# Kernel optimization log

Measured on AMD Instinct MI355X. Metric: run time of the kernel, lower is better.

Reference implementation:

```python
import jax, jax.numpy as jnp
import numpy as np

NUM_HEADS = 8
HEAD_DIM = 64
EMBED = NUM_HEADS * HEAD_DIM  # 512


def setup_inputs() -> dict:
    key = jax.random.key(0)
    ks = jax.random.split(key, 8)
    B, S = 4, 2048
    s = 1.0 / np.sqrt(HEAD_DIM)
    so = 1.0 / np.sqrt(EMBED)
    return {
        "queries": jax.random.normal(ks[0], (B, S, EMBED), jnp.float32),
        "keys": jax.random.normal(ks[1], (B, S, EMBED), jnp.float32),
        "values": jax.random.normal(ks[2], (B, S, EMBED), jnp.float32),
        "Wq": jax.random.uniform(ks[3], (HEAD_DIM, HEAD_DIM), jnp.float32, -s, s),
        "Wk": jax.random.uniform(ks[4], (HEAD_DIM, HEAD_DIM), jnp.float32, -s, s),
        "Wv": jax.random.uniform(ks[5], (HEAD_DIM, HEAD_DIM), jnp.float32, -s, s),
        "Wo": jax.random.uniform(ks[6], (EMBED, EMBED), jnp.float32, -so, so),
        "bo": jax.random.uniform(ks[7], (EMBED,), jnp.float32, -so, so),
    }


def reference(queries, keys, values, Wq, Wk, Wv, Wo, bo):
    B, Sq, _ = queries.shape
    # Faithful to source: keys/values are (buggily) reshaped from `queries`;
    # with equal seq lens this means k/v come from the queries tensor.
    q = queries.reshape(B, Sq, NUM_HEADS, HEAD_DIM)
    k = q
    v = q
    # per-head linear: torch Linear(x) = x @ W.T
    q = jnp.einsum('bshd,ed->bshe', q, Wq)
    k = jnp.einsum('bshd,ed->bshe', k, Wk)
    v = jnp.einsum('bshd,ed->bshe', v, Wv)
    sim = jnp.einsum('bqhd,bkhd->bhqk', q, k)  # [B,H,Sq,Sk]
    attn = jax.nn.softmax(sim * (1.0 / np.sqrt(HEAD_DIM)), axis=-1)
    out = jnp.einsum('bhqk,bkhd->bqhd', attn, v)
    out = out.reshape(B, Sq, EMBED)
    return out @ Wo.T + bo
```

## Files before the change

### kernel.cpp

```cpp
#include <hip/hip_runtime.h>
#include <cstddef>

#define S_ 2048
#define E_ 512
#define SPLIT_STRIDE 4194304u

typedef __attribute__((ext_vector_type(8)))  short bf16x8;
typedef __attribute__((ext_vector_type(16))) float f32x16;

__device__ __forceinline__ unsigned short f2bf(float f) {
    union { float f; unsigned u; } v; v.f = f;
    return (unsigned short)((v.u + 0x7FFFu + ((v.u >> 16) & 1u)) >> 16);
}
__device__ __forceinline__ unsigned pk2bf(float a, float b) {
    union { float f; unsigned u; } x, y; x.f = a; y.f = b;
    return __builtin_amdgcn_perm(y.u + 0x8000u, x.u + 0x8000u, 0x07060302u);
}
__device__ __forceinline__ float bflo(unsigned u) {
    union { unsigned u; float f; } v; v.u = u << 16; return v.f;
}
__device__ __forceinline__ float bfhi(unsigned u) {
    union { unsigned u; float f; } v; v.u = u & 0xffff0000u; return v.f;
}
__device__ __forceinline__ float fexp2(float x) {
#if __has_builtin(__builtin_amdgcn_exp2f)
    return __builtin_amdgcn_exp2f(x);
#else
    return exp2f(x);
#endif
}

__global__ __launch_bounds__(256) void prep_all(const float* __restrict__ X,
                                                const float* __restrict__ Wq,
                                                const float* __restrict__ Wk,
                                                const float* __restrict__ Wo,
                                                const float* __restrict__ Wv,
                                                unsigned short* __restrict__ Xbf,
                                                unsigned short* __restrict__ XTg,
                                                unsigned short* __restrict__ GT,
                                                unsigned short* __restrict__ W2) {
    __shared__ unsigned short T[64][72];
    const int bi = blockIdx.x, tid = threadIdx.x;
    if (bi < 1024) {
        const int st = bi & 31, h = (bi >> 5) & 7, b = bi >> 8;
        const int s0 = st * 64;
        const int j = tid >> 2, g = tid & 3;
        const float* src = X + ((size_t)(b * S_ + s0 + j) * E_) + h * 64 + g * 16;
        unsigned short us[16];
#pragma unroll
        for (int i = 0; i < 16; i += 4) {
            float4 f = *(const float4*)(src + i);
            us[i] = f2bf(f.x); us[i + 1] = f2bf(f.y);
            us[i + 2] = f2bf(f.z); us[i + 3] = f2bf(f.w);
        }
        size_t xb = ((size_t)(b * S_ + s0 + j) * E_) + h * 64 + g * 16;
        *(uint4*)&Xbf[xb]     = *(uint4*)&us[0];
        *(uint4*)&Xbf[xb + 8] = *(uint4*)&us[8];
#pragma unroll
        for (int i = 0; i < 16; ++i) T[g * 16 + i][j] = us[i];
        __syncthreads();
        const int d = tid >> 2;
        const int pm[16] = {0,1,2,3,8,9,10,11,4,5,6,7,12,13,14,15};
        unsigned short o[16];
#pragma unroll
        for (int i = 0; i < 16; ++i) o[i] = T[d][g * 16 + pm[i]];
        size_t tb = ((size_t)((b * 8 + h) * 64 + d)) * S_ + s0 + g * 16;
        *(uint4*)&XTg[tb]     = *(uint4*)&o[0];
        *(uint4*)&XTg[tb + 8] = *(uint4*)&o[8];
    } else if (bi < 1040) {
        int idx = (bi - 1024) * 256 + tid;
        int c = idx >> 6, d = idx & 63;
        float acc = 0.f;
#pragma unroll 8
        for (int e = 0; e < 64; ++e) acc += Wq[e * 64 + d] * Wk[e * 64 + c];
        GT[c * 64 + d] = f2bf(acc * 0.18033688011112042f);
    } else {
        int idx = (bi - 1040) * 256 + tid;
        int e = idx >> 9, f = idx & 511;
        int h = f >> 6, c = f & 63;
        const float* wo = Wo + e * 512 + h * 64;
        float acc = 0.f;
#pragma unroll 8
        for (int d = 0; d < 64; ++d) acc += wo[d] * Wv[d * 64 + c];
        W2[idx] = f2bf(acc);
    }
}

__global__ __launch_bounds__(256, 4) void attn_mfma(const unsigned short* __restrict__ Xbf,
                                                    const unsigned short* __restrict__ XTg,
                                                    const unsigned short* __restrict__ GT,
                                                    unsigned short* __restrict__ AOp,
                                                    float* __restrict__ Lp) {
    __shared__ union SM {
        unsigned short Q[128][72];
        unsigned short cbuf[2][2 * 64 * 72];
        unsigned short AOt[128][72];
    } sm;

    const int tid = threadIdx.x;
    const int w = tid >> 6, lane = tid & 63;
    const int lm = lane & 31, lh = lane >> 5;
    const int h = blockIdx.x & 7;
    const int rest = blockIdx.x >> 3;
    const int qt = rest & 15, b = (rest >> 4) & 3, split = rest >> 6;
    const int s0 = qt * 128, sk0 = split * (S_ / 2);

    {
        const int r = tid >> 1, c = (tid & 1) * 32;
        const unsigned short* src = Xbf + ((size_t)(b * S_ + s0 + r)) * E_ + h * 64 + c;
#pragma unroll
        for (int u = 0; u < 4; ++u) *(uint4*)&sm.Q[r][c + u * 8] = *(const uint4*)(src + u * 8);
    }
    __syncthreads();

    bf16x8 Ufrag[4];
    {
        f32x16 ua[2];
#pragma unroll
        for (int nt = 0; nt < 2; ++nt)
#pragma unroll
            for (int i = 0; i < 16; ++i) ua[nt][i] = 0.f;
#pragma unroll
        for (int ks = 0; ks < 4; ++ks) {
            bf16x8 aQ = *(const bf16x8*)&sm.Q[32 * w + lm][ks * 16 + lh * 8];
#pragma unroll
            for (int nt = 0; nt < 2; ++nt) {
                bf16x8 bG = *(const bf16x8*)&GT[(lm + 32 * nt) * 64 + ks * 16 + lh * 8];
                ua[nt] = __builtin_amdgcn_mfma_f32_32x32x16_bf16(aQ, bG, ua[nt], 0, 0, 0);
            }
        }
#pragma unroll
        for (int nt = 0; nt < 2; ++nt)
#pragma unroll
            for (int r = 0; r < 16; ++r)
                sm.Q[32 * w + (r & 3) + 8 * (r >> 2) + 4 * lh][lm + 32 * nt] = f2bf(ua[nt][r]);
#pragma unroll
        for (int ks = 0; ks < 4; ++ks)
            Ufrag[ks] = *(const bf16x8*)&sm.Q[32 * w + lm][ks * 16 + lh * 8];
    }
    __syncthreads();

    const int rr = tid >> 2, cc = (tid & 3) * 16;
    const unsigned short* srcX = Xbf + ((size_t)(b * S_ + rr)) * E_ + h * 64 + cc;
    const unsigned short* srcT = XTg + ((size_t)((b * 8 + h) * 64 + rr)) * S_ + cc;
    const int ldsOff = rr * 72 + cc;

    unsigned short* bufR = sm.cbuf[0];
    unsigned short* bufW = sm.cbuf[1];

    {
        const unsigned short* sx = srcX + (size_t)sk0 * E_;
        const unsigned short* st = srcT + sk0;
        *(uint4*)(bufR + ldsOff)               = *(const uint4*)sx;
        *(uint4*)(bufR + ldsOff + 8)           = *(const uint4*)(sx + 8);
        *(uint4*)(bufR + 64 * 72 + ldsOff)     = *(const uint4*)st;
        *(uint4*)(bufR + 64 * 72 + ldsOff + 8) = *(const uint4*)(st + 8);
    }
    __syncthreads();

    float lsum = 0.f;
    f32x16 AO[2];
#pragma unroll
    for (int mt = 0; mt < 2; ++mt)
#pragma unroll
        for (int i = 0; i < 16; ++i) AO[mt][i] = 0.f;

    for (int ck = 0; ck < 16; ++ck) {
        uint4 pre0, pre1, pre2, pre3;
        const bool have = (ck < 15);
        if (have) {
            const unsigned short* sx = srcX + (size_t)(sk0 + (ck + 1) * 64) * E_;
            const unsigned short* st = srcT + sk0 + (ck + 1) * 64;
            pre0 = *(const uint4*)sx;  pre1 = *(const uint4*)(sx + 8);
            pre2 = *(const uint4*)st;  pre3 = *(const uint4*)(st + 8);
        }

        f32x16 sc[2];
#pragma unroll
        for (int mt = 0; mt < 2; ++mt)
#pragma unroll
            for (int i = 0; i < 16; ++i) sc[mt][i] = 0.f;
#pragma unroll
        for (int ks = 0; ks < 4; ++ks)
#pragma unroll
            for (int mt = 0; mt < 2; ++mt) {
                bf16x8 aX = *(const bf16x8*)(bufR + (32 * mt + lm) * 72 + ks * 16 + lh * 8);
                sc[mt] = __builtin_amdgcn_mfma_f32_32x32x16_bf16(aX, Ufrag[ks], sc[mt], 0, 0, 0);
            }

#pragma unroll
        for (int js = 0; js < 4; ++js) {
            const int mt = js >> 1;
            union { unsigned u[4]; bf16x8 v; } bP;
#pragma unroll
            for (int i = 0; i < 4; ++i) {
                const int qq = 2 * (js & 1) + (i >> 1);
                float pa = fexp2(sc[mt][qq * 4 + 2 * (i & 1)]);
                float pb = fexp2(sc[mt][qq * 4 + 2 * (i & 1) + 1]);
                lsum += pa + pb;
                bP.u[i] = pk2bf(pa, pb);
            }
#pragma unroll
            for (int mtv = 0; mtv < 2; ++mtv) {
                bf16x8 aT = *(const bf16x8*)(bufR + 64 * 72 + (32 * mtv + lm) * 72 + js * 16 + lh * 8);
                AO[mtv] = __builtin_amdgcn_mfma_f32_32x32x16_bf16(aT, bP.v, AO[mtv], 0, 0, 0);
            }
        }

        if (have) {
            *(uint4*)(bufW + ldsOff)               = pre0;
            *(uint4*)(bufW + ldsOff + 8)           = pre1;
            *(uint4*)(bufW + 64 * 72 + ldsOff)     = pre2;
            *(uint4*)(bufW + 64 * 72 + ldsOff + 8) = pre3;
        }
        __syncthreads();
        unsigned short* t = bufR; bufR = bufW; bufW = t;
    }

    lsum += __shfl_xor(lsum, 32);
#pragma unroll
    for (int mt = 0; mt < 2; ++mt)
#pragma unroll
        for (int qq = 0; qq < 4; ++qq) {
            int d0 = 32 * mt + 8 * qq + 4 * lh;
            *(unsigned*)&sm.AOt[32 * w + lm][d0] =
                pk2bf(AO[mt][qq * 4 + 0], AO[mt][qq * 4 + 1]);
            *(unsigned*)&sm.AOt[32 * w + lm][d0 + 2] =
                pk2bf(AO[mt][qq * 4 + 2], AO[mt][qq * 4 + 3]);
        }
    __syncthreads();
    {
        const int r = tid >> 1, c = (tid & 1) * 32;
        unsigned short* dst = AOp + (size_t)split * SPLIT_STRIDE
                            + ((size_t)(b * S_ + s0 + r)) * E_ + h * 64 + c;
#pragma unroll
        for (int u = 0; u < 4; ++u)
            *(uint4*)(dst + u * 8) = *(const uint4*)&sm.AOt[r][c + u * 8];
    }
    if (lane < 32)
        Lp[((size_t)(split * 4 + b) * 8 + h) * S_ + s0 + 32 * w + lm] = lsum;
}

__global__ __launch_bounds__(256) void out_gemm_bf(const unsigned short* __restrict__ AOp,
                                                   const float* __restrict__ Lp,
                                                   const unsigned short* __restrict__ W2,
                                                   const float* __restrict__ bo,
                                                   float* __restrict__ out) {
    __shared__ unsigned short At[64][72];
    __shared__ unsigned short Bt[64][72];
    const int tid = threadIdx.x;
    const int w = tid >> 6, lane = tid & 63;
    const int lm = lane & 31, lh = lane >> 5;
    const int et = blockIdx.x & 7, rt = blockIdx.x >> 3;
    const int r0 = rt * 64, e0 = et * 64;
    const int rr = tid >> 2, cc = (tid & 3) * 16;
    const int srow = r0 + rr, bb = srow >> 11, ss = srow & 2047;

    f32x16 acc;
#pragma unroll
    for (int i = 0; i < 16; ++i) acc[i] = 0.f;

    for (int k0 = 0; k0 < 512; k0 += 64) {
        const int hh = k0 >> 6;
        const float linv = 1.0f / (Lp[((size_t)(bb)*8 + hh) * S_ + ss] +
                                   Lp[((size_t)(4 + bb) * 8 + hh) * S_ + ss]);
        __syncthreads();
        {
            const unsigned short* a0 = AOp + (size_t)srow * 512 + k0 + cc;
            const unsigned short* a1 = a0 + SPLIT_STRIDE;
            uint4 u0 = *(const uint4*)a0, u0b = *(const uint4*)(a0 + 8);
            uint4 u1 = *(const uint4*)a1, u1b = *(const uint4*)(a1 + 8);
            uint4 o, ob;
            o.x  = pk2bf((bflo(u0.x) + bflo(u1.x)) * linv, (bfhi(u0.x) + bfhi(u1.x)) * linv);
            o.y  = pk2bf((bflo(u0.y) + bflo(u1.y)) * linv, (bfhi(u0.y) + bfhi(u1.y)) * linv);
            o.z  = pk2bf((bflo(u0.z) + bflo(u1.z)) * linv, (bfhi(u0.z) + bfhi(u1.z)) * linv);
            o.w  = pk2bf((bflo(u0.w) + bflo(u1.w)) * linv, (bfhi(u0.w) + bfhi(u1.w)) * linv);
            ob.x = pk2bf((bflo(u0b.x) + bflo(u1b.x)) * linv, (bfhi(u0b.x) + bfhi(u1b.x)) * linv);
            ob.y = pk2bf((bflo(u0b.y) + bflo(u1b.y)) * linv, (bfhi(u0b.y) + bfhi(u1b.y)) * linv);
            ob.z = pk2bf((bflo(u0b.z) + bflo(u1b.z)) * linv, (bfhi(u0b.z) + bfhi(u1b.z)) * linv);
            ob.w = pk2bf((bflo(u0b.w) + bflo(u1b.w)) * linv, (bfhi(u0b.w) + bfhi(u1b.w)) * linv);
            *(uint4*)&At[rr][cc]     = o;
            *(uint4*)&At[rr][cc + 8] = ob;
            const unsigned short* sb = W2 + (size_t)(e0 + rr) * 512 + k0 + cc;
            *(uint4*)&Bt[rr][cc]     = *(const uint4*)sb;
            *(uint4*)&Bt[rr][cc + 8] = *(const uint4*)(sb + 8);
        }
        __syncthreads();
#pragma unroll
        for (int ks = 0; ks < 4; ++ks) {
            bf16x8 aA = *(const bf16x8*)&At[32 * (w & 1) + lm][ks * 16 + lh * 8];
            bf16x8 bW = *(const bf16x8*)&Bt[32 * (w >> 1) + lm][ks * 16 + lh * 8];
            acc = __builtin_amdgcn_mfma_f32_32x32x16_bf16(aA, bW, acc, 0, 0, 0);
        }
    }
    const float bv = bo[e0 + 32 * (w >> 1) + lm];
#pragma unroll
    for (int r = 0; r < 16; ++r) {
        int orow = r0 + 32 * (w & 1) + (r & 3) + 8 * (r >> 2) + 4 * lh;
        out[(size_t)orow * 512 + e0 + 32 * (w >> 1) + lm] = acc[r] + bv;
    }
}

extern "C" void kernel_launch(void* const* d_in, const int* in_sizes, int n_in,
                              void* d_out, int out_size, void* d_ws, size_t ws_size,
                              hipStream_t stream) {
    (void)in_sizes; (void)n_in; (void)out_size; (void)ws_size;
    const float* X  = (const float*)d_in[0];
    const float* Wq = (const float*)d_in[3];
    const float* Wk = (const float*)d_in[4];
    const float* Wv = (const float*)d_in[5];
    const float* Wo = (const float*)d_in[6];
    const float* bo = (const float*)d_in[7];

    float* ws = (float*)d_ws;
    unsigned short* W2bf = (unsigned short*)ws;
    unsigned short* GT   = (unsigned short*)(ws + 131072);
    unsigned short* Xbf  = (unsigned short*)(ws + 133120);
    unsigned short* XTg  = (unsigned short*)(ws + 2230272);
    unsigned short* AOp  = (unsigned short*)(ws + 4327424);
    float*          Lp   = ws + 8521728;

    prep_all   <<<2064, 256, 0, stream>>>(X, Wq, Wk, Wo, Wv, Xbf, XTg, GT, W2bf);
    attn_mfma  <<<1024, 256, 0, stream>>>(Xbf, XTg, GT, AOp, Lp);
    out_gemm_bf<<<1024, 256, 0, stream>>>(AOp, Lp, W2bf, bo, (float*)d_out);
}
```

Measured before the change: 170.0 us.

## Halve attention block to two waves each owning 64 query rows

The attention kernel now runs 128 threads per block, and each wave computes two 32-row query tiles instead of one. Each K/V fragment read from LDS feeds twice as many MFMAs, which halves LDS traffic per FLOP. The first key chunk is prefetched into registers while the query projection runs, and s_setprio is raised around the MFMA bursts. In exchange, register pressure roughly doubles (accumulators and Ufrag), which may reduce occupancy, and there are fewer waves to hide latency.

```diff
diff --git a/kernel.cpp b/kernel.cpp
--- a/kernel.cpp
+++ b/kernel.cpp
@@ -86,7 +86,7 @@
     }
 }
 
-__global__ __launch_bounds__(256, 4) void attn_mfma(const unsigned short* __restrict__ Xbf,
+__global__ __launch_bounds__(128, 2) void attn_mfma(const unsigned short* __restrict__ Xbf,
                                                     const unsigned short* __restrict__ XTg,
                                                     const unsigned short* __restrict__ GT,
                                                     unsigned short* __restrict__ AOp,
@@ -107,138 +107,184 @@
 
     {
         const int r = tid >> 1, c = (tid & 1) * 32;
-        const unsigned short* src = Xbf + ((size_t)(b * S_ + s0 + r)) * E_ + h * 64 + c;
-#pragma unroll
-        for (int u = 0; u < 4; ++u) *(uint4*)&sm.Q[r][c + u * 8] = *(const uint4*)(src + u * 8);
+#pragma unroll
+        for (int p = 0; p < 2; ++p) {
+            const unsigned short* src = Xbf + ((size_t)(b * S_ + s0 + 64 * p + r)) * E_ + h * 64 + c;
+#pragma unroll
+            for (int u = 0; u < 4; ++u)
+                *(uint4*)&sm.Q[64 * p + r][c + u * 8] = *(const uint4*)(src + u * 8);
+        }
     }
     __syncthreads();
 
-    bf16x8 Ufrag[4];
-    {
-        f32x16 ua[2];
-#pragma unroll
-        for (int nt = 0; nt < 2; ++nt)
-#pragma unroll
-            for (int i = 0; i < 16; ++i) ua[nt][i] = 0.f;
-#pragma unroll
-        for (int ks = 0; ks < 4; ++ks) {
-            bf16x8 aQ = *(const bf16x8*)&sm.Q[32 * w + lm][ks * 16 + lh * 8];
-#pragma unroll
-            for (int nt = 0; nt < 2; ++nt) {
-                bf16x8 bG = *(const bf16x8*)&GT[(lm + 32 * nt) * 64 + ks * 16 + lh * 8];
-                ua[nt] = __builtin_amdgcn_mfma_f32_32x32x16_bf16(aQ, bG, ua[nt], 0, 0, 0);
-            }
-        }
-#pragma unroll
-        for (int nt = 0; nt < 2; ++nt)
-#pragma unroll
-            for (int r = 0; r < 16; ++r)
-                sm.Q[32 * w + (r & 3) + 8 * (r >> 2) + 4 * lh][lm + 32 * nt] = f2bf(ua[nt][r]);
-#pragma unroll
-        for (int ks = 0; ks < 4; ++ks)
-            Ufrag[ks] = *(const bf16x8*)&sm.Q[32 * w + lm][ks * 16 + lh * 8];
-    }
-    __syncthreads();
-
-    const int rr = tid >> 2, cc = (tid & 3) * 16;
+    const int rr = tid >> 1, cc = (tid & 1) * 32;
     const unsigned short* srcX = Xbf + ((size_t)(b * S_ + rr)) * E_ + h * 64 + cc;
     const unsigned short* srcT = XTg + ((size_t)((b * 8 + h) * 64 + rr)) * S_ + cc;
     const int ldsOff = rr * 72 + cc;
 
+    uint4 pre[8];
+    {
+        const unsigned short* sx = srcX + (size_t)sk0 * E_;
+        const unsigned short* st = srcT + sk0;
+#pragma unroll
+        for (int u = 0; u < 4; ++u) pre[u]     = *(const uint4*)(sx + u * 8);
+#pragma unroll
+        for (int u = 0; u < 4; ++u) pre[4 + u] = *(const uint4*)(st + u * 8);
+    }
+
+    bf16x8 Ufrag[2][4];
+    {
+        f32x16 ua[2][2];
+#pragma unroll
+        for (int mt = 0; mt < 2; ++mt)
+#pragma unroll
+            for (int nt = 0; nt < 2; ++nt)
+#pragma unroll
+                for (int i = 0; i < 16; ++i) ua[mt][nt][i] = 0.f;
+#pragma unroll
+        for (int ks = 0; ks < 4; ++ks) {
+            bf16x8 bG0 = *(const bf16x8*)&GT[(lm +  0) * 64 + ks * 16 + lh * 8];
+            bf16x8 bG1 = *(const bf16x8*)&GT[(lm + 32) * 64 + ks * 16 + lh * 8];
+#pragma unroll
+            for (int mt = 0; mt < 2; ++mt) {
+                bf16x8 aQ = *(const bf16x8*)&sm.Q[64 * w + 32 * mt + lm][ks * 16 + lh * 8];
+                ua[mt][0] = __builtin_amdgcn_mfma_f32_32x32x16_bf16(aQ, bG0, ua[mt][0], 0, 0, 0);
+                ua[mt][1] = __builtin_amdgcn_mfma_f32_32x32x16_bf16(aQ, bG1, ua[mt][1], 0, 0, 0);
+            }
+        }
+#pragma unroll
+        for (int mt = 0; mt < 2; ++mt)
+#pragma unroll
+            for (int nt = 0; nt < 2; ++nt)
+#pragma unroll
+                for (int r = 0; r < 16; ++r)
+                    sm.Q[64 * w + 32 * mt + (r & 3) + 8 * (r >> 2) + 4 * lh][lm + 32 * nt] =
+                        f2bf(ua[mt][nt][r]);
+#pragma unroll
+        for (int g = 0; g < 2; ++g)
+#pragma unroll
+            for (int ks = 0; ks < 4; ++ks)
+                Ufrag[g][ks] = *(const bf16x8*)&sm.Q[64 * w + 32 * g + lm][ks * 16 + lh * 8];
+    }
+    __syncthreads();
+
     unsigned short* bufR = sm.cbuf[0];
     unsigned short* bufW = sm.cbuf[1];
 
     {
-        const unsigned short* sx = srcX + (size_t)sk0 * E_;
-        const unsigned short* st = srcT + sk0;
-        *(uint4*)(bufR + ldsOff)               = *(const uint4*)sx;
-        *(uint4*)(bufR + ldsOff + 8)           = *(const uint4*)(sx + 8);
-        *(uint4*)(bufR + 64 * 72 + ldsOff)     = *(const uint4*)st;
-        *(uint4*)(bufR + 64 * 72 + ldsOff + 8) = *(const uint4*)(st + 8);
+#pragma unroll
+        for (int u = 0; u < 4; ++u) *(uint4*)(bufR + ldsOff + u * 8)           = pre[u];
+#pragma unroll
+        for (int u = 0; u < 4; ++u) *(uint4*)(bufR + 64 * 72 + ldsOff + u * 8) = pre[4 + u];
     }
     __syncthreads();
 
-    float lsum = 0.f;
-    f32x16 AO[2];
+    float lsum0 = 0.f, lsum1 = 0.f;
+    f32x16 AO[2][2];
 #pragma unroll
     for (int mt = 0; mt < 2; ++mt)
 #pragma unroll
-        for (int i = 0; i < 16; ++i) AO[mt][i] = 0.f;
+        for (int nt = 0; nt < 2; ++nt)
+#pragma unroll
+            for (int i = 0; i < 16; ++i) AO[mt][nt][i] = 0.f;
 
     for (int ck = 0; ck < 16; ++ck) {
-        uint4 pre0, pre1, pre2, pre3;
         const bool have = (ck < 15);
         if (have) {
             const unsigned short* sx = srcX + (size_t)(sk0 + (ck + 1) * 64) * E_;
             const unsigned short* st = srcT + sk0 + (ck + 1) * 64;
-            pre0 = *(const uint4*)sx;  pre1 = *(const uint4*)(sx + 8);
-            pre2 = *(const uint4*)st;  pre3 = *(const uint4*)(st + 8);
-        }
-
-        f32x16 sc[2];
+#pragma unroll
+            for (int u = 0; u < 4; ++u) pre[u]     = *(const uint4*)(sx + u * 8);
+#pragma unroll
+            for (int u = 0; u < 4; ++u) pre[4 + u] = *(const uint4*)(st + u * 8);
+        }
+
+        f32x16 sc[2][2];
 #pragma unroll
         for (int mt = 0; mt < 2; ++mt)
 #pragma unroll
-            for (int i = 0; i < 16; ++i) sc[mt][i] = 0.f;
+            for (int nt = 0; nt < 2; ++nt)
+#pragma unroll
+                for (int i = 0; i < 16; ++i) sc[mt][nt][i] = 0.f;
+        __builtin_amdgcn_s_setprio(1);
 #pragma unroll
         for (int ks = 0; ks < 4; ++ks)
 #pragma unroll
             for (int mt = 0; mt < 2; ++mt) {
                 bf16x8 aX = *(const bf16x8*)(bufR + (32 * mt + lm) * 72 + ks * 16 + lh * 8);
-                sc[mt] = __builtin_amdgcn_mfma_f32_32x32x16_bf16(aX, Ufrag[ks], sc[mt], 0, 0, 0);
-            }
+                sc[mt][0] = __builtin_amdgcn_mfma_f32_32x32x16_bf16(aX, Ufrag[0][ks], sc[mt][0], 0, 0, 0);
+                sc[mt][1] = __builtin_amdgcn_mfma_f32_32x32x16_bf16(aX, Ufrag[1][ks], sc[mt][1], 0, 0, 0);
+            }
+        __builtin_amdgcn_s_setprio(0);
 
 #pragma unroll
         for (int js = 0; js < 4; ++js) {
             const int mt = js >> 1;
-            union { unsigned u[4]; bf16x8 v; } bP;
+            union { unsigned u[4]; bf16x8 v; } bP0, bP1;
 #pragma unroll
             for (int i = 0; i < 4; ++i) {
                 const int qq = 2 * (js & 1) + (i >> 1);
-                float pa = fexp2(sc[mt][qq * 4 + 2 * (i & 1)]);
-                float pb = fexp2(sc[mt][qq * 4 + 2 * (i & 1) + 1]);
-                lsum += pa + pb;
-                bP.u[i] = pk2bf(pa, pb);
-            }
+                float pa = fexp2(sc[mt][0][qq * 4 + 2 * (i & 1)]);
+                float pb = fexp2(sc[mt][0][qq * 4 + 2 * (i & 1) + 1]);
+                lsum0 += pa + pb;
+                bP0.u[i] = pk2bf(pa, pb);
+                float pc = fexp2(sc[mt][1][qq * 4 + 2 * (i & 1)]);
+                float pd = fexp2(sc[mt][1][qq * 4 + 2 * (i & 1) + 1]);
+                lsum1 += pc + pd;
+                bP1.u[i] = pk2bf(pc, pd);
+            }
+            __builtin_amdgcn_s_setprio(1);
 #pragma unroll
             for (int mtv = 0; mtv < 2; ++mtv) {
                 bf16x8 aT = *(const bf16x8*)(bufR + 64 * 72 + (32 * mtv + lm) * 72 + js * 16 + lh * 8);
-                AO[mtv] = __builtin_amdgcn_mfma_f32_32x32x16_bf16(aT, bP.v, AO[mtv], 0, 0, 0);
-            }
+                AO[mtv][0] = __builtin_amdgcn_mfma_f32_32x32x16_bf16(aT, bP0.v, AO[mtv][0], 0, 0, 0);
+                AO[mtv][1] = __builtin_amdgcn_mfma_f32_32x32x16_bf16(aT, bP1.v, AO[mtv][1], 0, 0, 0);
+            }
+            __builtin_amdgcn_s_setprio(0);
         }
 
         if (have) {
-            *(uint4*)(bufW + ldsOff)               = pre0;
-            *(uint4*)(bufW + ldsOff + 8)           = pre1;
-            *(uint4*)(bufW + 64 * 72 + ldsOff)     = pre2;
-            *(uint4*)(bufW + 64 * 72 + ldsOff + 8) = pre3;
+#pragma unroll
+            for (int u = 0; u < 4; ++u) *(uint4*)(bufW + ldsOff + u * 8)           = pre[u];
+#pragma unroll
+            for (int u = 0; u < 4; ++u) *(uint4*)(bufW + 64 * 72 + ldsOff + u * 8) = pre[4 + u];
         }
         __syncthreads();
         unsigned short* t = bufR; bufR = bufW; bufW = t;
     }
 
-    lsum += __shfl_xor(lsum, 32);
-#pragma unroll
-    for (int mt = 0; mt < 2; ++mt)
-#pragma unroll
-        for (int qq = 0; qq < 4; ++qq) {
-            int d0 = 32 * mt + 8 * qq + 4 * lh;
-            *(unsigned*)&sm.AOt[32 * w + lm][d0] =
-                pk2bf(AO[mt][qq * 4 + 0], AO[mt][qq * 4 + 1]);
-            *(unsigned*)&sm.AOt[32 * w + lm][d0 + 2] =
-                pk2bf(AO[mt][qq * 4 + 2], AO[mt][qq * 4 + 3]);
-        }
+    lsum0 += __shfl_xor(lsum0, 32);
+    lsum1 += __shfl_xor(lsum1, 32);
+#pragma unroll
+    for (int mtv = 0; mtv < 2; ++mtv)
+#pragma unroll
+        for (int nt = 0; nt < 2; ++nt)
+#pragma unroll
+            for (int qq = 0; qq < 4; ++qq) {
+                const int d0 = 32 * mtv + 8 * qq + 4 * lh;
+                const int row = 64 * w + 32 * nt + lm;
+                *(unsigned*)&sm.AOt[row][d0] =
+                    pk2bf(AO[mtv][nt][qq * 4 + 0], AO[mtv][nt][qq * 4 + 1]);
+                *(unsigned*)&sm.AOt[row][d0 + 2] =
+                    pk2bf(AO[mtv][nt][qq * 4 + 2], AO[mtv][nt][qq * 4 + 3]);
+            }
     __syncthreads();
     {
         const int r = tid >> 1, c = (tid & 1) * 32;
-        unsigned short* dst = AOp + (size_t)split * SPLIT_STRIDE
-                            + ((size_t)(b * S_ + s0 + r)) * E_ + h * 64 + c;
-#pragma unroll
-        for (int u = 0; u < 4; ++u)
-            *(uint4*)(dst + u * 8) = *(const uint4*)&sm.AOt[r][c + u * 8];
-    }
-    if (lane < 32)
-        Lp[((size_t)(split * 4 + b) * 8 + h) * S_ + s0 + 32 * w + lm] = lsum;
+#pragma unroll
+        for (int p = 0; p < 2; ++p) {
+            unsigned short* dst = AOp + (size_t)split * SPLIT_STRIDE
+                                + ((size_t)(b * S_ + s0 + 64 * p + r)) * E_ + h * 64 + c;
+#pragma unroll
+            for (int u = 0; u < 4; ++u)
+                *(uint4*)(dst + u * 8) = *(const uint4*)&sm.AOt[64 * p + r][c + u * 8];
+        }
+    }
+    if (lane < 32) {
+        const size_t lb = ((size_t)(split * 4 + b) * 8 + h) * S_ + s0 + 64 * w;
+        Lp[lb + lm]      = lsum0;
+        Lp[lb + 32 + lm] = lsum1;
+    }
 }
 
 __global__ __launch_bounds__(256) void out_gemm_bf(const unsigned short* __restrict__ AOp,
@@ -321,6 +367,6 @@
     float*          Lp   = ws + 8521728;
 
     prep_all   <<<2064, 256, 0, stream>>>(X, Wq, Wk, Wo, Wv, Xbf, XTg, GT, W2bf);
-    attn_mfma  <<<1024, 256, 0, stream>>>(Xbf, XTg, GT, AOp, Lp);
+    attn_mfma  <<<1024, 128, 0, stream>>>(Xbf, XTg, GT, AOp, Lp);
     out_gemm_bf<<<1024, 256, 0, stream>>>(AOp, Lp, W2bf, bo, (float*)d_out);
 }
```

New measurement: 200.9 us. +18.2%, slower.
